# Kernel tuning notes

Hardware: AMD Instinct MI355X
Metric: run time of the kernel (lower is better)

## Reference

```python
import jax, jax.numpy as jnp
import numpy as np

DIM = 512
D_STATE = 16
D_CONV = 4
EXPAND = 2
D_INNER = EXPAND * DIM          # 1024
DT_RANK = (DIM + D_STATE - 1) // D_STATE  # 32
B_SZ, L_SEQ = 2, 2048


def layer_norm(x, w, b, eps=1e-5):
    mu = jnp.mean(x, axis=-1, keepdims=True)
    var = jnp.mean(jnp.square(x - mu), axis=-1, keepdims=True)
    return (x - mu) * jax.lax.rsqrt(var + eps) * w + b


def setup_inputs() -> dict:
    key = jax.random.key(0)
    ks = jax.random.split(key, 12)
    x = jax.random.normal(ks[0], (B_SZ, DIM, L_SEQ), dtype=jnp.float32)
    # LayerNorms init to weight=1, bias=0 per _init_weights
    norm1_w = jnp.ones((DIM,), jnp.float32)
    norm1_b = jnp.zeros((DIM,), jnp.float32)
    norm2_w = jnp.ones((DIM,), jnp.float32)
    norm2_b = jnp.zeros((DIM,), jnp.float32)
    # Mamba params (Linear weights trunc-normal std=0.02 per _init_weights; bias=0)
    in_proj_w = 0.02 * jax.random.truncated_normal(ks[1], -2., 2., (2 * D_INNER, DIM), jnp.float32)
    conv_w = 0.1 * jax.random.normal(ks[2], (D_INNER, D_CONV), jnp.float32)
    conv_b = jnp.zeros((D_INNER,), jnp.float32)
    x_proj_w = 0.02 * jax.random.truncated_normal(ks[3], -2., 2., (DT_RANK + 2 * D_STATE, D_INNER), jnp.float32)
    dt_proj_w = 0.02 * jax.random.truncated_normal(ks[4], -2., 2., (D_INNER, DT_RANK), jnp.float32)
    # dt bias: inverse-softplus of dt ~ U(1e-3, 0.1), standard Mamba init
    dt = jnp.exp(jax.random.uniform(ks[5], (D_INNER,), jnp.float32) * (np.log(0.1) - np.log(1e-3)) + np.log(1e-3))
    dt_proj_b = dt + jnp.log(-jnp.expm1(-dt))
    # S4D-real init: A = diag(1..d_state), stored as log
    A_log = jnp.log(jnp.broadcast_to(jnp.arange(1, D_STATE + 1, dtype=jnp.float32), (D_INNER, D_STATE)))
    D = jnp.ones((D_INNER,), jnp.float32)
    out_proj_w = 0.02 * jax.random.truncated_normal(ks[6], -2., 2., (DIM, D_INNER), jnp.float32)
    return {"x": x, "norm1_w": norm1_w, "norm1_b": norm1_b, "norm2_w": norm2_w,
            "norm2_b": norm2_b, "in_proj_w": in_proj_w, "conv_w": conv_w, "conv_b": conv_b,
            "x_proj_w": x_proj_w, "dt_proj_w": dt_proj_w, "dt_proj_b": dt_proj_b,
            "A_log": A_log, "D": D, "out_proj_w": out_proj_w}


def mamba_block(xn, in_proj_w, conv_w, conv_b, x_proj_w, dt_proj_w, dt_proj_b, A_log, D, out_proj_w):
    # xn: [B, L, dim]
    Bb, Ll, _ = xn.shape
    di = in_proj_w.shape[0] // 2
    xz = jnp.einsum('bld,ed->ble', xn, in_proj_w)          # [B, L, 2*di]
    x_in, z = xz[..., :di], xz[..., di:]
    # depthwise causal conv1d over L
    K = conv_w.shape[1]
    xp = jnp.pad(x_in, ((0, 0), (K - 1, 0), (0, 0)))
    xc = sum(xp[:, k:k + Ll, :] * conv_w[:, k] for k in range(K)) + conv_b
    xc = jax.nn.silu(xc)                                    # [B, L, di]
    # input-dependent dt, B, C
    dbl = jnp.einsum('bld,ed->ble', xc, x_proj_w)
    R, N = dt_proj_w.shape[1], A_log.shape[1]
    dt_lo, Bm, Cm = dbl[..., :R], dbl[..., R:R + N], dbl[..., R + N:]
    dt = jax.nn.softplus(jnp.einsum('blr,dr->bld', dt_lo, dt_proj_w) + dt_proj_b)  # [B, L, di]
    A = -jnp.exp(A_log)                                     # [di, N]
    dA = jnp.exp(jnp.einsum('bld,dn->bldn', dt, A))         # [B, L, di, N]
    dBu = jnp.einsum('bld,bln,bld->bldn', dt, Bm, xc)       # dt * B * u
    def step(h, inp):
        dA_t, dBu_t, C_t = inp                              # [B,di,N], [B,di,N], [B,N]
        h = dA_t * h + dBu_t
        y = jnp.einsum('bdn,bn->bd', h, C_t)
        return h, y
    h0 = jnp.zeros((Bb, di, N), xn.dtype)
    _, ys = jax.lax.scan(step, h0, (jnp.swapaxes(dA, 0, 1), jnp.swapaxes(dBu, 0, 1), jnp.swapaxes(Cm, 0, 1)))
    y = jnp.swapaxes(ys, 0, 1)                              # [B, L, di]
    y = y + xc * D
    y = y * jax.nn.silu(z)
    return jnp.einsum('ble,de->bld', y, out_proj_w)         # [B, L, dim]


def reference(x, norm1_w, norm1_b, norm2_w, norm2_b, in_proj_w, conv_w, conv_b,
              x_proj_w, dt_proj_w, dt_proj_b, A_log, D, out_proj_w):
    # x: [B, C, L]
    xf = jnp.swapaxes(x, 1, 2)                              # [B, L, C]
    xn = layer_norm(xf, norm1_w, norm1_b)
    xm = mamba_block(xn, in_proj_w, conv_w, conv_b, x_proj_w,
                     dt_proj_w, dt_proj_b, A_log, D, out_proj_w)
    out = layer_norm(xf + xm, norm2_w, norm2_b)
    return jnp.swapaxes(out, 1, 2)                          # [B, C, L]
```

## Files before the change

kernel.cpp:

```cpp
#include <hip/hip_runtime.h>
#include <math.h>

#define BSZ 2
#define LSEQ 2048
#define DMODEL 512
#define DINNER 1024
#define NST 16
#define RDT 32
#define GDBL 64
#define NCH 16
#define CHL 128
#define LOG2E 1.4426950408889634f

typedef unsigned short u16;
typedef unsigned int   u32;
typedef __attribute__((ext_vector_type(8))) __bf16 bf16x8;
typedef __attribute__((ext_vector_type(4))) float  f32x4;

__device__ __forceinline__ float siluf(float x){ return x / (1.f + __expf(-x)); }
__device__ __forceinline__ float softplusf(float x){
  return (x > 20.f) ? x : log1pf(__expf(x));
}
__device__ __forceinline__ u16 f2bf(float f){
  u32 u = __float_as_uint(f);
  u += 0x7fff + ((u >> 16) & 1);
  return (u16)(u >> 16);
}
__device__ __forceinline__ float bf2f(u16 u){ return __uint_as_float((u32)u << 16); }
__device__ __forceinline__ float exp2fast(float x){
  float r; asm("v_exp_f32 %0, %1" : "=v"(r) : "v"(x)); return r;
}
__device__ __forceinline__ void gld16(const void* g, void* l){
  __builtin_amdgcn_global_load_lds((const __attribute__((address_space(1))) void*)g,
                                   (__attribute__((address_space(3))) void*)l, 16, 0, 0);
}

__global__ void k0_wcvt(const float* __restrict__ Wip, const float* __restrict__ Wop,
                        const float* __restrict__ Wxp, const float* __restrict__ Wdt,
                        u16* __restrict__ wipb, u16* __restrict__ wopb,
                        u16* __restrict__ wxpb, u16* __restrict__ wdtb){
  int idx = blockIdx.x*256 + threadIdx.x;
  int i4 = idx * 4;
  const float* src; u16* dst;
  if (i4 < 1048576){ src = Wip + i4; dst = wipb + i4; }
  else if (i4 < 1048576 + 524288){ int j = i4 - 1048576; src = Wop + j; dst = wopb + j; }
  else if (i4 < 1048576 + 524288 + 65536){ int j = i4 - 1048576 - 524288; src = Wxp + j; dst = wxpb + j; }
  else { int j = i4 - 1048576 - 524288 - 65536; if (j >= 32768) return; src = Wdt + j; dst = wdtb + j; }
  float4 v = *(const float4*)src;
  u32 lo = (u32)f2bf(v.x) | ((u32)f2bf(v.y) << 16);
  u32 hi = (u32)f2bf(v.z) | ((u32)f2bf(v.w) << 16);
  *(uint2*)dst = make_uint2(lo, hi);
}

__global__ void k1_ln_norm(const float* __restrict__ x, const float* __restrict__ w1,
                           const float* __restrict__ b1, u16* __restrict__ xnb){
  int blk = blockIdx.x;
  int b = blk >> 6;
  int l0 = (blk & 63) * 32;
  int t = threadIdx.x;
  int lc = t & 31, dc = t >> 5;
  const float* xb = x + (size_t)b*DMODEL*LSEQ;
  float s=0.f, q=0.f;
  for (int d = dc*64; d < dc*64+64; ++d){
    float v = xb[d*LSEQ + l0 + lc];
    s += v; q += v*v;
  }
  __shared__ float ss[8][33], qq[8][33];
  __shared__ float muL[32], rsL[32];
  ss[dc][lc]=s; qq[dc][lc]=q;
  __syncthreads();
  if (t < 32){
    float S=0.f,Q=0.f;
    for (int i=0;i<8;++i){S+=ss[i][t];Q+=qq[i][t];}
    float m = S/DMODEL;
    muL[t]=m; rsL[t]=rsqrtf(Q/DMODEL - m*m + 1e-5f);
  }
  __syncthreads();
  float mu = muL[lc], rs = rsL[lc];
  u16* orow = xnb + ((size_t)(b*LSEQ + l0 + lc))*DMODEL;
  for (int d = dc*64; d < dc*64+64; d += 2){
    float v0 = (xb[d*LSEQ + l0 + lc]     - mu)*rs*w1[d]   + b1[d];
    float v1 = (xb[(d+1)*LSEQ + l0 + lc] - mu)*rs*w1[d+1] + b1[d+1];
    *(u32*)&orow[d] = (u32)f2bf(v0) | ((u32)f2bf(v1) << 16);
  }
}

__global__ __launch_bounds__(256) void k2_inproj_mfma(
    const u16* __restrict__ xnb, const u16* __restrict__ wipb,
    u16* __restrict__ xinb, u16* __restrict__ zb){
  __shared__ u16 As[2][4096];
  __shared__ u16 Bs[2][4096];
  int t = threadIdx.x;
  int wid = t >> 6, lane = t & 63;
  int n0 = blockIdx.x * 128, m0 = blockIdx.y * 128;
  int wr = wid >> 1, wc = wid & 1;
  int lr = lane & 15, q = lane >> 4;

  const u16* gA = xnb  + (size_t)(m0 + (t>>2))*DMODEL + (t&3)*8;
  const u16* gB = wipb + (size_t)(n0 + (t>>2))*DMODEL + (t&3)*8;

  f32x4 acc[4][4];
  #pragma unroll
  for (int i=0;i<4;++i)
    #pragma unroll
    for (int j=0;j<4;++j) acc[i][j] = (f32x4){0.f,0.f,0.f,0.f};

  #pragma unroll
  for (int r=0;r<2;++r){
    gld16(gA + (size_t)r*64*DMODEL, &As[0][(wid*64 + r*256)*8]);
    gld16(gB + (size_t)r*64*DMODEL, &Bs[0][(wid*64 + r*256)*8]);
  }
  const int abase = (wr*64 + lr)*32 + q*8;
  const int bbase = (wc*64 + lr)*32 + q*8;

  for (int ks = 0; ks < 16; ++ks){
    int cur = ks & 1;
    __syncthreads();
    if (ks < 15){
      const u16* gA2 = gA + (ks+1)*32;
      const u16* gB2 = gB + (ks+1)*32;
      #pragma unroll
      for (int r=0;r<2;++r){
        gld16(gA2 + (size_t)r*64*DMODEL, &As[cur^1][(wid*64 + r*256)*8]);
        gld16(gB2 + (size_t)r*64*DMODEL, &Bs[cur^1][(wid*64 + r*256)*8]);
      }
    }
    bf16x8 a[4], bv[4];
    #pragma unroll
    for (int mf=0; mf<4; ++mf) a[mf]  = *(const bf16x8*)&As[cur][abase + mf*512];
    #pragma unroll
    for (int nf=0; nf<4; ++nf) bv[nf] = *(const bf16x8*)&Bs[cur][bbase + nf*512];
    #pragma unroll
    for (int mf=0; mf<4; ++mf)
      #pragma unroll
      for (int nf=0; nf<4; ++nf)
        acc[mf][nf] = __builtin_amdgcn_mfma_f32_16x16x32_bf16(a[mf], bv[nf], acc[mf][nf], 0, 0, 0);
  }

  bool half = (n0 >= DINNER);
  u16* outp = half ? zb : xinb;
  int colb = (half ? n0 - DINNER : n0) + wc*64 + lr;
  #pragma unroll
  for (int mf=0; mf<4; ++mf){
    int rowb = m0 + wr*64 + mf*16 + q*4;
    #pragma unroll
    for (int nf=0; nf<4; ++nf){
      f32x4 v = acc[mf][nf];
      int col = colb + nf*16;
      #pragma unroll
      for (int j=0;j<4;++j) outp[(size_t)(rowb+j)*DINNER + col] = f2bf(v[j]);
    }
  }
}

__global__ void k3_conv(const u16* __restrict__ xinb, const float* __restrict__ cw,
                        const float* __restrict__ cb, u16* __restrict__ xc){
  int idx = blockIdx.x*blockDim.x + threadIdx.x;
  int e4 = (idx & (DINNER/4 - 1)) * 4;
  int m = idx >> 8;
  int b = m >> 11; int l = m & (LSEQ-1);
  float4 accb = *(const float4*)&cb[e4];
  float acc[4] = {accb.x, accb.y, accb.z, accb.w};
  #pragma unroll
  for (int k=0;k<4;++k){
    int li = l + k - 3;
    if (li >= 0){
      ushort4 v = *(const ushort4*)&xinb[((size_t)(b*LSEQ+li))*DINNER + e4];
      acc[0] += bf2f(v.x) * cw[(e4+0)*4 + k];
      acc[1] += bf2f(v.y) * cw[(e4+1)*4 + k];
      acc[2] += bf2f(v.z) * cw[(e4+2)*4 + k];
      acc[3] += bf2f(v.w) * cw[(e4+3)*4 + k];
    }
  }
  u32 lo = (u32)f2bf(siluf(acc[0])) | ((u32)f2bf(siluf(acc[1])) << 16);
  u32 hi = (u32)f2bf(siluf(acc[2])) | ((u32)f2bf(siluf(acc[3])) << 16);
  *(uint2*)&xc[(size_t)m*DINNER + e4] = make_uint2(lo, hi);
}

__global__ __launch_bounds__(256) void k4_xproj_mfma(
    const u16* __restrict__ xcbf, const u16* __restrict__ wxpb,
    float* __restrict__ dbl, u16* __restrict__ dtlob){
  __shared__ u16 As[2][4096];
  __shared__ u16 Bs[2][4096];
  int t = threadIdx.x;
  int wid = t >> 6, lane = t & 63;
  int m0 = blockIdx.x * 64;
  int wr = wid >> 1, wc = wid & 1;
  int lr = lane & 15, q = lane >> 4;

  const u16* gA = xcbf + (size_t)(m0 + (t>>2))*DINNER + (t&3)*8;
  const u16* gB = wxpb + (size_t)(t>>2)*DINNER + (t&3)*8;

  f32x4 acc[2][2];
  #pragma unroll
  for (int i=0;i<2;++i)
    #pragma unroll
    for (int j=0;j<2;++j) acc[i][j] = (f32x4){0.f,0.f,0.f,0.f};

  #pragma unroll
  for (int r=0;r<2;++r){
    gld16(gA + r*32, &As[0][(r*256 + wid*64)*8]);
    gld16(gB + r*32, &Bs[0][(r*256 + wid*64)*8]);
  }
  const int abase = (wr*32 + lr)*32 + q*8;
  const int bbase = (wc*32 + lr)*32 + q*8;

  for (int ks = 0; ks < 16; ++ks){
    int cur = ks & 1;
    __syncthreads();
    if (ks < 15){
      const u16* gA2 = gA + (ks+1)*64;
      const u16* gB2 = gB + (ks+1)*64;
      #pragma unroll
      for (int r=0;r<2;++r){
        gld16(gA2 + r*32, &As[cur^1][(r*256 + wid*64)*8]);
        gld16(gB2 + r*32, &Bs[cur^1][(r*256 + wid*64)*8]);
      }
    }
    bf16x8 a[2][2], bv[2][2];
    #pragma unroll
    for (int mf=0; mf<2; ++mf)
      #pragma unroll
      for (int s=0; s<2; ++s) a[mf][s] = *(const bf16x8*)&As[cur][abase + mf*512 + s*2048];
    #pragma unroll
    for (int nf=0; nf<2; ++nf)
      #pragma unroll
      for (int s=0; s<2; ++s) bv[nf][s] = *(const bf16x8*)&Bs[cur][bbase + nf*512 + s*2048];
    #pragma unroll
    for (int s=0; s<2; ++s)
      #pragma unroll
      for (int mf=0; mf<2; ++mf)
        #pragma unroll
        for (int nf=0; nf<2; ++nf)
          acc[mf][nf] = __builtin_amdgcn_mfma_f32_16x16x32_bf16(a[mf][s], bv[nf][s], acc[mf][nf], 0, 0, 0);
  }

  #pragma unroll
  for (int mf=0; mf<2; ++mf){
    int rowb = m0 + wr*32 + mf*16 + q*4;
    #pragma unroll
    for (int nf=0; nf<2; ++nf){
      f32x4 v = acc[mf][nf];
      int col = wc*32 + nf*16 + lr;
      #pragma unroll
      for (int j=0;j<4;++j) dbl[(size_t)(rowb+j)*GDBL + col] = v[j];
      if (wc == 0){
        #pragma unroll
        for (int j=0;j<4;++j) dtlob[(size_t)(rowb+j)*RDT + col] = f2bf(v[j]);
      }
    }
  }
}

__global__ __launch_bounds__(256) void k5_dtproj_mfma(
    const u16* __restrict__ dtlob, const u16* __restrict__ wdtb,
    const float* __restrict__ dtbias, u16* __restrict__ dtb){
  __shared__ u16 As[2048];
  __shared__ u16 Bs[2048];
  int t = threadIdx.x;
  int wid = t >> 6, lane = t & 63;
  int m0 = blockIdx.x * 64, d0 = blockIdx.y * 64;
  int wr = wid >> 1, wc = wid & 1;
  int lr = lane & 15, q = lane >> 4;

  gld16(dtlob + (size_t)(m0 + (t>>2))*RDT + (t&3)*8, &As[wid*512]);
  gld16(wdtb  + (size_t)(d0 + (t>>2))*RDT + (t&3)*8, &Bs[wid*512]);
  __syncthreads();

  f32x4 acc[2][2];
  bf16x8 a[2], bv[2];
  #pragma unroll
  for (int mf=0; mf<2; ++mf) a[mf]  = *(const bf16x8*)&As[(wr*32 + mf*16 + lr)*32 + q*8];
  #pragma unroll
  for (int nf=0; nf<2; ++nf) bv[nf] = *(const bf16x8*)&Bs[(wc*32 + nf*16 + lr)*32 + q*8];
  #pragma unroll
  for (int mf=0; mf<2; ++mf)
    #pragma unroll
    for (int nf=0; nf<2; ++nf)
      acc[mf][nf] = __builtin_amdgcn_mfma_f32_16x16x32_bf16(a[mf], bv[nf], (f32x4){0.f,0.f,0.f,0.f}, 0, 0, 0);

  #pragma unroll
  for (int nf=0; nf<2; ++nf){
    int col = d0 + wc*32 + nf*16 + lr;
    float bias = dtbias[col];
    #pragma unroll
    for (int mf=0; mf<2; ++mf){
      int rowb = m0 + wr*32 + mf*16 + q*4;
      f32x4 v = acc[mf][nf];
      #pragma unroll
      for (int j=0;j<4;++j) dtb[(size_t)(rowb+j)*DINNER + col] = f2bf(softplusf(v[j] + bias));
    }
  }
}

__global__ __launch_bounds__(256) void k6a_pass1(
    const float* __restrict__ dblg, const u16* __restrict__ xcg, const u16* __restrict__ dtg,
    const float* __restrict__ Alog,
    float* __restrict__ hend, float* __restrict__ dchunk){
  int blk = blockIdx.x;
  int b = blk >> 10;
  int slice = (blk >> 4) & 63;
  int chunk = blk & 15;
  int d0 = slice * 16;
  int t = threadIdx.x;
  int dl = t >> 4, n = t & 15;
  int d = d0 + dl;
  float Adn2 = -__expf(Alog[d*NST + n]) * LOG2E;
  float h = 0.f;
  float S = 0.f;

  __shared__ float dts_t[16][36];
  __shared__ float xcs_t[16][36];
  __shared__ float Bts[16][36];

  for (int sub = 0; sub < CHL/32; ++sub){
    int l0 = chunk*CHL + sub*32;
    __syncthreads();
    {
      int c = t & 15;
      int r1 = t >> 4, r2 = r1 + 16;
      size_t row1 = (size_t)(b*LSEQ + l0 + r1);
      size_t row2 = (size_t)(b*LSEQ + l0 + r2);
      dts_t[c][r1] = bf2f(dtg[row1*DINNER + d0 + c]);
      dts_t[c][r2] = bf2f(dtg[row2*DINNER + d0 + c]);
      xcs_t[c][r1] = bf2f(xcg[row1*DINNER + d0 + c]);
      xcs_t[c][r2] = bf2f(xcg[row2*DINNER + d0 + c]);
      Bts[c][r1]   = dblg[row1*GDBL + RDT + c];
      Bts[c][r2]   = dblg[row2*GDBL + RDT + c];
    }
    __syncthreads();
    for (int r0=0; r0<32; r0+=4){
      float4 dt4 = *(const float4*)&dts_t[dl][r0];
      float4 xc4 = *(const float4*)&xcs_t[dl][r0];
      float4 B4  = *(const float4*)&Bts[n][r0];
      const float* dtp = (const float*)&dt4;
      const float* xcp = (const float*)&xc4;
      const float* Bp  = (const float*)&B4;
      #pragma unroll
      for (int j=0;j<4;++j){
        float dtv = dtp[j];
        float a = exp2fast(dtv * Adn2);
        h = a*h + (dtv * xcp[j]) * Bp[j];
        S += dtv;
      }
    }
  }
  int cix = ((b*NCH + chunk)*DINNER + d)*NST + n;
  hend[cix]   = h;
  dchunk[cix] = exp2fast(Adn2 * S);
}

__global__ __launch_bounds__(256) void k6c_pass2(
    const float* __restrict__ dblg, const u16* __restrict__ xcg, const u16* __restrict__ zg,
    const u16* __restrict__ dtg,
    const float* __restrict__ Alog, const float* __restrict__ Dp,
    const float* __restrict__ hend, const float* __restrict__ dchk,
    u16* __restrict__ ybf){
  int blk = blockIdx.x;
  int b = blk >> 10;
  int slice = (blk >> 4) & 63;
  int chunk = blk & 15;
  int d0 = slice * 16;
  int t = threadIdx.x;
  int dl = t >> 4, n = t & 15;
  int d = d0 + dl;
  float Adn2 = -__expf(Alog[d*NST + n]) * LOG2E;

  float h = 0.f;
  {
    size_t base = ((size_t)(b*NCH) << 14) + (d<<4) + n;
    for (int c = 0; c < chunk; ++c){
      size_t ix = base + ((size_t)c << 14);
      h = dchk[ix]*h + hend[ix];
    }
  }

  __shared__ float dts_t[16][36];
  __shared__ float xcs_t[16][36];
  __shared__ float Bts[16][36];
  __shared__ float Cts[16][36];
  __shared__ float zs[32][17];
  __shared__ float ys[16][33];
  __shared__ float Dps[16];
  __shared__ float pbuf[32][260];

  if (t < 16) Dps[t] = Dp[d0+t];

  for (int sub = 0; sub < CHL/32; ++sub){
    int l0 = chunk*CHL + sub*32;
    __syncthreads();
    {
      int c = t & 15;
      int r1 = t >> 4, r2 = r1 + 16;
      size_t row1 = (size_t)(b*LSEQ + l0 + r1);
      size_t row2 = (size_t)(b*LSEQ + l0 + r2);
      dts_t[c][r1] = bf2f(dtg[row1*DINNER + d0 + c]);
      dts_t[c][r2] = bf2f(dtg[row2*DINNER + d0 + c]);
      xcs_t[c][r1] = bf2f(xcg[row1*DINNER + d0 + c]);
      xcs_t[c][r2] = bf2f(xcg[row2*DINNER + d0 + c]);
      Bts[c][r1]   = dblg[row1*GDBL + RDT + c];
      Bts[c][r2]   = dblg[row2*GDBL + RDT + c];
      Cts[c][r1]   = dblg[row1*GDBL + RDT + NST + c];
      Cts[c][r2]   = dblg[row2*GDBL + RDT + NST + c];
      zs[r1][c]    = bf2f(zg[row1*DINNER + d0 + c]);
      zs[r2][c]    = bf2f(zg[row2*DINNER + d0 + c]);
    }
    __syncthreads();
    for (int r0=0; r0<32; r0+=4){
      float4 dt4 = *(const float4*)&dts_t[dl][r0];
      float4 xc4 = *(const float4*)&xcs_t[dl][r0];
      float4 B4  = *(const float4*)&Bts[n][r0];
      float4 C4  = *(const float4*)&Cts[n][r0];
      const float* dtp = (const float*)&dt4;
      const float* xcp = (const float*)&xc4;
      const float* Bp  = (const float*)&B4;
      const float* Cp  = (const float*)&C4;
      #pragma unroll
      for (int j=0;j<4;++j){
        int r = r0 + j;
        float dtv = dtp[j];
        float a = exp2fast(dtv * Adn2);
        h = a*h + (dtv * xcp[j]) * Bp[j];
        pbuf[r][t ^ ((r&1)<<4)] = h * Cp[j];
      }
    }
    __syncthreads();
    {
      int rr_ = t & 31, dd_ = t >> 5;
      #pragma unroll
      for (int pp=0; pp<2; ++pp){
        int dd = dd_ + pp*8;
        int x0 = (dd*16) ^ ((rr_&1)<<4);
        float4 v0 = *(const float4*)&pbuf[rr_][x0 + 0];
        float4 v1 = *(const float4*)&pbuf[rr_][x0 + 4];
        float4 v2 = *(const float4*)&pbuf[rr_][x0 + 8];
        float4 v3 = *(const float4*)&pbuf[rr_][x0 + 12];
        float sum = (((v0.x+v0.y)+(v0.z+v0.w)) + ((v1.x+v1.y)+(v1.z+v1.w)))
                  + (((v2.x+v2.y)+(v2.z+v2.w)) + ((v3.x+v3.y)+(v3.z+v3.w)));
        float xv = xcs_t[dd][rr_];
        float zv = zs[rr_][dd];
        ys[dd][rr_] = (sum + xv*Dps[dd]) * siluf(zv);
      }
    }
    __syncthreads();
    {
      int r = t >> 3, pr = t & 7;
      float v0 = ys[pr*2][r];
      float v1 = ys[pr*2+1][r];
      u32 u = (u32)f2bf(v0) | ((u32)f2bf(v1) << 16);
      *(u32*)&ybf[((size_t)(b*LSEQ + l0 + r))*DINNER + d0 + pr*2] = u;
    }
  }
}

__global__ __launch_bounds__(256) void k7_outproj_mfma(
    const u16* __restrict__ ybf, const u16* __restrict__ wopb, float* __restrict__ xmT){
  __shared__ u16 As[2][4096];
  __shared__ u16 Bs[2][4096];
  int t = threadIdx.x;
  int wid = t >> 6, lane = t & 63;
  int n0 = blockIdx.x * 64, m0 = blockIdx.y * 64;
  int b  = m0 >> 11;
  int l0 = m0 & (LSEQ-1);
  int wr = wid >> 1, wc = wid & 1;
  int lr = lane & 15, q = lane >> 4;

  const u16* gA = ybf  + (size_t)(m0 + (t>>2))*DINNER + (t&3)*8;
  const u16* gB = wopb + (size_t)(n0 + (t>>2))*DINNER + (t&3)*8;

  f32x4 acc[2][2];
  #pragma unroll
  for (int i=0;i<2;++i)
    #pragma unroll
    for (int j=0;j<2;++j) acc[i][j] = (f32x4){0.f,0.f,0.f,0.f};

  #pragma unroll
  for (int r=0;r<2;++r){
    gld16(gA + r*32, &As[0][(r*256 + wid*64)*8]);
    gld16(gB + r*32, &Bs[0][(r*256 + wid*64)*8]);
  }
  const int abase = (wr*32 + lr)*32 + q*8;
  const int bbase = (wc*32 + lr)*32 + q*8;

  for (int ks = 0; ks < 16; ++ks){
    int cur = ks & 1;
    __syncthreads();
    if (ks < 15){
      const u16* gA2 = gA + (ks+1)*64;
      const u16* gB2 = gB + (ks+1)*64;
      #pragma unroll
      for (int r=0;r<2;++r){
        gld16(gA2 + r*32, &As[cur^1][(r*256 + wid*64)*8]);
        gld16(gB2 + r*32, &Bs[cur^1][(r*256 + wid*64)*8]);
      }
    }
    bf16x8 a[2][2], bv[2][2];
    #pragma unroll
    for (int mf=0; mf<2; ++mf)
      #pragma unroll
      for (int s=0; s<2; ++s) a[mf][s] = *(const bf16x8*)&As[cur][abase + mf*512 + s*2048];
    #pragma unroll
    for (int nf=0; nf<2; ++nf)
      #pragma unroll
      for (int s=0; s<2; ++s) bv[nf][s] = *(const bf16x8*)&Bs[cur][bbase + nf*512 + s*2048];
    #pragma unroll
    for (int s=0; s<2; ++s)
      #pragma unroll
      for (int mf=0; mf<2; ++mf)
        #pragma unroll
        for (int nf=0; nf<2; ++nf)
          acc[mf][nf] = __builtin_amdgcn_mfma_f32_16x16x32_bf16(a[mf][s], bv[nf][s], acc[mf][nf], 0, 0, 0);
  }

  #pragma unroll
  for (int mf=0; mf<2; ++mf){
    int lrow = l0 + wr*32 + mf*16 + q*4;
    #pragma unroll
    for (int nf=0; nf<2; ++nf){
      f32x4 v = acc[mf][nf];
      int col = n0 + wc*32 + nf*16 + lr;
      *(float4*)&xmT[((size_t)(b*DMODEL + col))*LSEQ + lrow] = make_float4(v[0],v[1],v[2],v[3]);
    }
  }
}

__global__ void k8_fused(const float* __restrict__ x, const float* __restrict__ xmT,
                         const float* __restrict__ w2, const float* __restrict__ b2,
                         float* __restrict__ out){
  int blk = blockIdx.x;
  int b = blk >> 7;
  int l0 = (blk & 127) * 16;
  int t = threadIdx.x;
  int lc = t & 15, dc = t >> 4;
  const float* xb = x   + (size_t)b*DMODEL*LSEQ + l0 + lc;
  const float* xt = xmT + (size_t)b*DMODEL*LSEQ + l0 + lc;
  float s=0.f, q=0.f;
  for (int d = dc*32; d < dc*32+32; ++d){
    float v = xb[d*LSEQ] + xt[d*LSEQ];
    s += v; q += v*v;
  }
  __shared__ float ss[16][17], qq[16][17];
  __shared__ float muL[16], rsL[16];
  ss[dc][lc]=s; qq[dc][lc]=q;
  __syncthreads();
  if (t < 16){
    float S=0.f,Q=0.f;
    for (int i=0;i<16;++i){S+=ss[i][t];Q+=qq[i][t];}
    float m = S/DMODEL;
    muL[t]=m; rsL[t]=rsqrtf(Q/DMODEL - m*m + 1e-5f);
  }
  __syncthreads();
  float mu = muL[lc], rs = rsL[lc];
  float* ob = out + (size_t)b*DMODEL*LSEQ + l0 + lc;
  for (int d = dc*32; d < dc*32+32; ++d){
    float v = xb[d*LSEQ] + xt[d*LSEQ];
    ob[d*LSEQ] = (v - mu)*rs*w2[d] + b2[d];
  }
}

extern "C" void kernel_launch(void* const* d_in, const int* in_sizes, int n_in,
                              void* d_out, int out_size, void* d_ws, size_t ws_size,
                              hipStream_t stream) {
  const float* x      = (const float*)d_in[0];
  const float* n1w    = (const float*)d_in[1];
  const float* n1b    = (const float*)d_in[2];
  const float* n2w    = (const float*)d_in[3];
  const float* n2b    = (const float*)d_in[4];
  const float* Wip    = (const float*)d_in[5];
  const float* cw     = (const float*)d_in[6];
  const float* cb     = (const float*)d_in[7];
  const float* Wxp    = (const float*)d_in[8];
  const float* Wdt    = (const float*)d_in[9];
  const float* dtbias = (const float*)d_in[10];
  const float* Alog   = (const float*)d_in[11];
  const float* Dp     = (const float*)d_in[12];
  const float* Wop    = (const float*)d_in[13];
  float* out = (float*)d_out;

  float* ws = (float*)d_ws;
  size_t o = 0;
  u16*  xinb = (u16*)(ws + o); o += 2097152;
  u16*  zb   = (u16*)(ws + o); o += 2097152;
  u16*  xcb  = (u16*)(ws + o); o += 2097152;
  u16*  ybf  = (u16*)(ws + o); o += 2097152;
  u16*  dtb  = (u16*)(ws + o); o += 2097152;
  u16*  xnb  = (u16*)(ws + o); o += 1048576;
  u16*  wipb = (u16*)(ws + o); o += 524288;
  u16*  wopb = (u16*)(ws + o); o += 262144;
  u16*  wxpb = (u16*)(ws + o); o += 32768;
  u16*  wdtb = (u16*)(ws + o); o += 16384;
  u16*  dtlob= (u16*)(ws + o); o += 65536;
  float* dbl  = ws + o; o += 262144;
  float* hend = ws + o; o += 524288;
  float* dchk = ws + o; o += 524288;
  float* xmT  = ws + o; o += 2097152;

  k0_wcvt      <<<dim3(1632),        dim3(256), 0, stream>>>(Wip, Wop, Wxp, Wdt, wipb, wopb, wxpb, wdtb);
  k1_ln_norm   <<<dim3(BSZ*64),      dim3(256), 0, stream>>>(x, n1w, n1b, xnb);
  k2_inproj_mfma<<<dim3(16,32),      dim3(256), 0, stream>>>(xnb, wipb, xinb, zb);
  k3_conv      <<<dim3(4096),        dim3(256), 0, stream>>>(xinb, cw, cb, xcb);
  k4_xproj_mfma<<<dim3(64),          dim3(256), 0, stream>>>(xcb, wxpb, dbl, dtlob);
  k5_dtproj_mfma<<<dim3(64,16),      dim3(256), 0, stream>>>(dtlob, wdtb, dtbias, dtb);
  k6a_pass1    <<<dim3(BSZ*64*NCH),  dim3(256), 0, stream>>>(dbl, xcb, dtb, Alog, hend, dchk);
  k6c_pass2    <<<dim3(BSZ*64*NCH),  dim3(256), 0, stream>>>(dbl, xcb, zb, dtb, Alog, Dp, hend, dchk, ybf);
  k7_outproj_mfma<<<dim3(8,64),      dim3(256), 0, stream>>>(ybf, wopb, xmT);
  k8_fused     <<<dim3(BSZ*128),     dim3(256), 0, stream>>>(x, xmT, n2w, n2b, out);
}
```

Baseline: 182.8 us.

## Remap selective scan to four states per thread with vectorized loads and DPP reduction

The two chunked-scan kernels now give each thread four state channels for one inner channel and cover 64 channels per block instead of 16. Chunk length is halved, so there are twice as many chunks. Tiles are loaded as 16-byte bf16 vectors into row-major shared memory. The C-weighted sum over states is reduced with DPP quad shuffles instead of a large shared partial-sum buffer, and the output is written as vectorized bf16. This aims to cut transposed scalar global loads, shared-memory traffic and barriers per step. In exchange, the serial cross-chunk carry loop in pass 2 gets longer and the hend/dchk buffers double in size.

New measurement: 165.1 us. 9.6% less time.

```diff
diff --git a/kernel.cpp b/kernel.cpp
--- a/kernel.cpp
+++ b/kernel.cpp
@@ -8,8 +8,8 @@
 #define NST 16
 #define RDT 32
 #define GDBL 64
-#define NCH 16
-#define CHL 128
+#define NCH 32
+#define CHL 64
 #define LOG2E 1.4426950408889634f
 
 typedef unsigned short u16;
@@ -33,6 +33,17 @@
 __device__ __forceinline__ void gld16(const void* g, void* l){
   __builtin_amdgcn_global_load_lds((const __attribute__((address_space(1))) void*)g,
                                    (__attribute__((address_space(3))) void*)l, 16, 0, 0);
+}
+__device__ __forceinline__ void unpack8(uint4 v, float* f){
+  f[0]=__uint_as_float(v.x<<16); f[1]=__uint_as_float(v.x&0xffff0000u);
+  f[2]=__uint_as_float(v.y<<16); f[3]=__uint_as_float(v.y&0xffff0000u);
+  f[4]=__uint_as_float(v.z<<16); f[5]=__uint_as_float(v.z&0xffff0000u);
+  f[6]=__uint_as_float(v.w<<16); f[7]=__uint_as_float(v.w&0xffff0000u);
+}
+__device__ __forceinline__ float quadsum(float p){
+  p += __int_as_float(__builtin_amdgcn_update_dpp(0, __float_as_int(p), 0xB1, 0xf, 0xf, true));
+  p += __int_as_float(__builtin_amdgcn_update_dpp(0, __float_as_int(p), 0x4E, 0xf, 0xf, true));
+  return p;
 }
 
 __global__ void k0_wcvt(const float* __restrict__ Wip, const float* __restrict__ Wop,
@@ -298,56 +309,62 @@
     const float* __restrict__ Alog,
     float* __restrict__ hend, float* __restrict__ dchunk){
   int blk = blockIdx.x;
-  int b = blk >> 10;
-  int slice = (blk >> 4) & 63;
-  int chunk = blk & 15;
-  int d0 = slice * 16;
-  int t = threadIdx.x;
-  int dl = t >> 4, n = t & 15;
-  int d = d0 + dl;
-  float Adn2 = -__expf(Alog[d*NST + n]) * LOG2E;
-  float h = 0.f;
-  float S = 0.f;
-
-  __shared__ float dts_t[16][36];
-  __shared__ float xcs_t[16][36];
-  __shared__ float Bts[16][36];
+  int b = blk >> 9;
+  int dblk = (blk >> 5) & 15;
+  int chunk = blk & 31;
+  int d0 = dblk * 64;
+  int t = threadIdx.x;
+  int d = t >> 2, ng = t & 3;
+
+  float4 Adn2;
+  {
+    float4 al = *(const float4*)&Alog[(d0+d)*NST + ng*4];
+    Adn2.x = -__expf(al.x)*LOG2E; Adn2.y = -__expf(al.y)*LOG2E;
+    Adn2.z = -__expf(al.z)*LOG2E; Adn2.w = -__expf(al.w)*LOG2E;
+  }
+  float h0=0.f, h1=0.f, h2=0.f, h3=0.f, S=0.f;
+
+  __shared__ float dts[32][64];
+  __shared__ float xcs[32][64];
+  __shared__ float Bst[32][16];
 
   for (int sub = 0; sub < CHL/32; ++sub){
     int l0 = chunk*CHL + sub*32;
     __syncthreads();
     {
-      int c = t & 15;
-      int r1 = t >> 4, r2 = r1 + 16;
-      size_t row1 = (size_t)(b*LSEQ + l0 + r1);
-      size_t row2 = (size_t)(b*LSEQ + l0 + r2);
-      dts_t[c][r1] = bf2f(dtg[row1*DINNER + d0 + c]);
-      dts_t[c][r2] = bf2f(dtg[row2*DINNER + d0 + c]);
-      xcs_t[c][r1] = bf2f(xcg[row1*DINNER + d0 + c]);
-      xcs_t[c][r2] = bf2f(xcg[row2*DINNER + d0 + c]);
-      Bts[c][r1]   = dblg[row1*GDBL + RDT + c];
-      Bts[c][r2]   = dblg[row2*GDBL + RDT + c];
-    }
-    __syncthreads();
-    for (int r0=0; r0<32; r0+=4){
-      float4 dt4 = *(const float4*)&dts_t[dl][r0];
-      float4 xc4 = *(const float4*)&xcs_t[dl][r0];
-      float4 B4  = *(const float4*)&Bts[n][r0];
-      const float* dtp = (const float*)&dt4;
-      const float* xcp = (const float*)&xc4;
-      const float* Bp  = (const float*)&B4;
-      #pragma unroll
-      for (int j=0;j<4;++j){
-        float dtv = dtp[j];
-        float a = exp2fast(dtv * Adn2);
-        h = a*h + (dtv * xcp[j]) * Bp[j];
-        S += dtv;
+      int r = t >> 3, c8 = t & 7;
+      size_t row = (size_t)(b*LSEQ + l0 + r);
+      uint4 dv = *(const uint4*)&dtg[row*DINNER + d0 + c8*8];
+      uint4 xv = *(const uint4*)&xcg[row*DINNER + d0 + c8*8];
+      float df[8], xf[8];
+      unpack8(dv, df); unpack8(xv, xf);
+      *(float4*)&dts[r][c8*8]   = make_float4(df[0],df[1],df[2],df[3]);
+      *(float4*)&dts[r][c8*8+4] = make_float4(df[4],df[5],df[6],df[7]);
+      *(float4*)&xcs[r][c8*8]   = make_float4(xf[0],xf[1],xf[2],xf[3]);
+      *(float4*)&xcs[r][c8*8+4] = make_float4(xf[4],xf[5],xf[6],xf[7]);
+      if (t < 128){
+        int rB = t >> 2, qB = t & 3;
+        *(float4*)&Bst[rB][qB*4] = *(const float4*)&dblg[((size_t)(b*LSEQ + l0 + rB))*GDBL + RDT + qB*4];
       }
     }
-  }
-  int cix = ((b*NCH + chunk)*DINNER + d)*NST + n;
-  hend[cix]   = h;
-  dchunk[cix] = exp2fast(Adn2 * S);
+    __syncthreads();
+    #pragma unroll 4
+    for (int r = 0; r < 32; ++r){
+      float dtv = dts[r][d];
+      float xcv = xcs[r][d];
+      float4 Bv = *(const float4*)&Bst[r][ng*4];
+      float u = dtv * xcv;
+      h0 = exp2fast(dtv*Adn2.x)*h0 + u*Bv.x;
+      h1 = exp2fast(dtv*Adn2.y)*h1 + u*Bv.y;
+      h2 = exp2fast(dtv*Adn2.z)*h2 + u*Bv.z;
+      h3 = exp2fast(dtv*Adn2.w)*h3 + u*Bv.w;
+      S += dtv;
+    }
+  }
+  size_t cix = ((size_t)(b*NCH + chunk)*DINNER + d0 + d)*NST + ng*4;
+  *(float4*)&hend[cix]   = make_float4(h0, h1, h2, h3);
+  *(float4*)&dchunk[cix] = make_float4(exp2fast(Adn2.x*S), exp2fast(Adn2.y*S),
+                                       exp2fast(Adn2.z*S), exp2fast(Adn2.w*S));
 }
 
 __global__ __launch_bounds__(256) void k6c_pass2(
@@ -357,98 +374,98 @@
     const float* __restrict__ hend, const float* __restrict__ dchk,
     u16* __restrict__ ybf){
   int blk = blockIdx.x;
-  int b = blk >> 10;
-  int slice = (blk >> 4) & 63;
-  int chunk = blk & 15;
-  int d0 = slice * 16;
-  int t = threadIdx.x;
-  int dl = t >> 4, n = t & 15;
-  int d = d0 + dl;
-  float Adn2 = -__expf(Alog[d*NST + n]) * LOG2E;
-
-  float h = 0.f;
+  int b = blk >> 9;
+  int dblk = (blk >> 5) & 15;
+  int chunk = blk & 31;
+  int d0 = dblk * 64;
+  int t = threadIdx.x;
+  int d = t >> 2, ng = t & 3;
+
+  float4 Adn2;
   {
-    size_t base = ((size_t)(b*NCH) << 14) + (d<<4) + n;
+    float4 al = *(const float4*)&Alog[(d0+d)*NST + ng*4];
+    Adn2.x = -__expf(al.x)*LOG2E; Adn2.y = -__expf(al.y)*LOG2E;
+    Adn2.z = -__expf(al.z)*LOG2E; Adn2.w = -__expf(al.w)*LOG2E;
+  }
+
+  float h0=0.f, h1=0.f, h2=0.f, h3=0.f;
+  {
+    size_t base = ((size_t)(b*NCH)*DINNER + d0 + d)*NST + ng*4;
     for (int c = 0; c < chunk; ++c){
-      size_t ix = base + ((size_t)c << 14);
-      h = dchk[ix]*h + hend[ix];
-    }
-  }
-
-  __shared__ float dts_t[16][36];
-  __shared__ float xcs_t[16][36];
-  __shared__ float Bts[16][36];
-  __shared__ float Cts[16][36];
-  __shared__ float zs[32][17];
-  __shared__ float ys[16][33];
-  __shared__ float Dps[16];
-  __shared__ float pbuf[32][260];
-
-  if (t < 16) Dps[t] = Dp[d0+t];
+      size_t ix = base + (size_t)c*DINNER*NST;
+      float4 hv = *(const float4*)&hend[ix];
+      float4 dv = *(const float4*)&dchk[ix];
+      h0 = dv.x*h0 + hv.x; h1 = dv.y*h1 + hv.y;
+      h2 = dv.z*h2 + hv.z; h3 = dv.w*h3 + hv.w;
+    }
+  }
+
+  __shared__ float dts[32][64];
+  __shared__ float xcs[32][64];
+  __shared__ float BCs[32][32];
+  __shared__ float ys[32][64];
+  __shared__ float Dps[64];
+
+  if (t < 64) Dps[t] = Dp[d0 + t];
 
   for (int sub = 0; sub < CHL/32; ++sub){
     int l0 = chunk*CHL + sub*32;
     __syncthreads();
     {
-      int c = t & 15;
-      int r1 = t >> 4, r2 = r1 + 16;
-      size_t row1 = (size_t)(b*LSEQ + l0 + r1);
-      size_t row2 = (size_t)(b*LSEQ + l0 + r2);
-      dts_t[c][r1] = bf2f(dtg[row1*DINNER + d0 + c]);
-      dts_t[c][r2] = bf2f(dtg[row2*DINNER + d0 + c]);
-      xcs_t[c][r1] = bf2f(xcg[row1*DINNER + d0 + c]);
-      xcs_t[c][r2] = bf2f(xcg[row2*DINNER + d0 + c]);
-      Bts[c][r1]   = dblg[row1*GDBL + RDT + c];
-      Bts[c][r2]   = dblg[row2*GDBL + RDT + c];
-      Cts[c][r1]   = dblg[row1*GDBL + RDT + NST + c];
-      Cts[c][r2]   = dblg[row2*GDBL + RDT + NST + c];
-      zs[r1][c]    = bf2f(zg[row1*DINNER + d0 + c]);
-      zs[r2][c]    = bf2f(zg[row2*DINNER + d0 + c]);
-    }
-    __syncthreads();
-    for (int r0=0; r0<32; r0+=4){
-      float4 dt4 = *(const float4*)&dts_t[dl][r0];
-      float4 xc4 = *(const float4*)&xcs_t[dl][r0];
-      float4 B4  = *(const float4*)&Bts[n][r0];
-      float4 C4  = *(const float4*)&Cts[n][r0];
-      const float* dtp = (const float*)&dt4;
-      const float* xcp = (const float*)&xc4;
-      const float* Bp  = (const float*)&B4;
-      const float* Cp  = (const float*)&C4;
-      #pragma unroll
-      for (int j=0;j<4;++j){
-        int r = r0 + j;
-        float dtv = dtp[j];
-        float a = exp2fast(dtv * Adn2);
-        h = a*h + (dtv * xcp[j]) * Bp[j];
-        pbuf[r][t ^ ((r&1)<<4)] = h * Cp[j];
-      }
+      int r = t >> 3, c8 = t & 7;
+      size_t row = (size_t)(b*LSEQ + l0 + r);
+      uint4 dv = *(const uint4*)&dtg[row*DINNER + d0 + c8*8];
+      uint4 xv = *(const uint4*)&xcg[row*DINNER + d0 + c8*8];
+      float df[8], xf[8];
+      unpack8(dv, df); unpack8(xv, xf);
+      *(float4*)&dts[r][c8*8]   = make_float4(df[0],df[1],df[2],df[3]);
+      *(float4*)&dts[r][c8*8+4] = make_float4(df[4],df[5],df[6],df[7]);
+      *(float4*)&xcs[r][c8*8]   = make_float4(xf[0],xf[1],xf[2],xf[3]);
+      *(float4*)&xcs[r][c8*8+4] = make_float4(xf[4],xf[5],xf[6],xf[7]);
+      *(float4*)&BCs[r][c8*4]   = *(const float4*)&dblg[row*GDBL + RDT + c8*4];
+    }
+    __syncthreads();
+    #pragma unroll 4
+    for (int r = 0; r < 32; ++r){
+      float dtv = dts[r][d];
+      float xcv = xcs[r][d];
+      float4 Bv = *(const float4*)&BCs[r][ng*4];
+      float4 Cv = *(const float4*)&BCs[r][16 + ng*4];
+      float u = dtv * xcv;
+      h0 = exp2fast(dtv*Adn2.x)*h0 + u*Bv.x;
+      h1 = exp2fast(dtv*Adn2.y)*h1 + u*Bv.y;
+      h2 = exp2fast(dtv*Adn2.z)*h2 + u*Bv.z;
+      h3 = exp2fast(dtv*Adn2.w)*h3 + u*Bv.w;
+      float p = h0*Cv.x + h1*Cv.y + h2*Cv.z + h3*Cv.w;
+      p = quadsum(p);
+      if (ng == 0) ys[r][d] = p;
     }
     __syncthreads();
     {
-      int rr_ = t & 31, dd_ = t >> 5;
-      #pragma unroll
-      for (int pp=0; pp<2; ++pp){
-        int dd = dd_ + pp*8;
-        int x0 = (dd*16) ^ ((rr_&1)<<4);
-        float4 v0 = *(const float4*)&pbuf[rr_][x0 + 0];
-        float4 v1 = *(const float4*)&pbuf[rr_][x0 + 4];
-        float4 v2 = *(const float4*)&pbuf[rr_][x0 + 8];
-        float4 v3 = *(const float4*)&pbuf[rr_][x0 + 12];
-        float sum = (((v0.x+v0.y)+(v0.z+v0.w)) + ((v1.x+v1.y)+(v1.z+v1.w)))
-                  + (((v2.x+v2.y)+(v2.z+v2.w)) + ((v3.x+v3.y)+(v3.z+v3.w)));
-        float xv = xcs_t[dd][rr_];
-        float zv = zs[rr_][dd];
-        ys[dd][rr_] = (sum + xv*Dps[dd]) * siluf(zv);
-      }
-    }
-    __syncthreads();
-    {
-      int r = t >> 3, pr = t & 7;
-      float v0 = ys[pr*2][r];
-      float v1 = ys[pr*2+1][r];
-      u32 u = (u32)f2bf(v0) | ((u32)f2bf(v1) << 16);
-      *(u32*)&ybf[((size_t)(b*LSEQ + l0 + r))*DINNER + d0 + pr*2] = u;
+      int r = t >> 3, c8 = t & 7;
+      size_t row = (size_t)(b*LSEQ + l0 + r);
+      uint4 zv = *(const uint4*)&zg[row*DINNER + d0 + c8*8];
+      float zf[8]; unpack8(zv, zf);
+      float4 s0 = *(const float4*)&ys[r][c8*8];
+      float4 s1 = *(const float4*)&ys[r][c8*8+4];
+      float4 x0 = *(const float4*)&xcs[r][c8*8];
+      float4 x1 = *(const float4*)&xcs[r][c8*8+4];
+      float4 D0 = *(const float4*)&Dps[c8*8];
+      float4 D1 = *(const float4*)&Dps[c8*8+4];
+      float y0 = (s0.x + x0.x*D0.x)*siluf(zf[0]);
+      float y1 = (s0.y + x0.y*D0.y)*siluf(zf[1]);
+      float y2 = (s0.z + x0.z*D0.z)*siluf(zf[2]);
+      float y3 = (s0.w + x0.w*D0.w)*siluf(zf[3]);
+      float y4 = (s1.x + x1.x*D1.x)*siluf(zf[4]);
+      float y5 = (s1.y + x1.y*D1.y)*siluf(zf[5]);
+      float y6 = (s1.z + x1.z*D1.z)*siluf(zf[6]);
+      float y7 = (s1.w + x1.w*D1.w)*siluf(zf[7]);
+      uint4 o;
+      o.x = (u32)f2bf(y0) | ((u32)f2bf(y1) << 16);
+      o.y = (u32)f2bf(y2) | ((u32)f2bf(y3) << 16);
+      o.z = (u32)f2bf(y4) | ((u32)f2bf(y5) << 16);
+      o.w = (u32)f2bf(y6) | ((u32)f2bf(y7) << 16);
+      *(uint4*)&ybf[row*DINNER + d0 + c8*8] = o;
     }
   }
 }
@@ -591,8 +608,8 @@
   u16*  wdtb = (u16*)(ws + o); o += 16384;
   u16*  dtlob= (u16*)(ws + o); o += 65536;
   float* dbl  = ws + o; o += 262144;
-  float* hend = ws + o; o += 524288;
-  float* dchk = ws + o; o += 524288;
+  float* hend = ws + o; o += 1048576;
+  float* dchk = ws + o; o += 1048576;
   float* xmT  = ws + o; o += 2097152;
 
   k0_wcvt      <<<dim3(1632),        dim3(256), 0, stream>>>(Wip, Wop, Wxp, Wdt, wipb, wopb, wxpb, wdtb);
@@ -601,8 +618,8 @@
   k3_conv      <<<dim3(4096),        dim3(256), 0, stream>>>(xinb, cw, cb, xcb);
   k4_xproj_mfma<<<dim3(64),          dim3(256), 0, stream>>>(xcb, wxpb, dbl, dtlob);
   k5_dtproj_mfma<<<dim3(64,16),      dim3(256), 0, stream>>>(dtlob, wdtb, dtbias, dtb);
-  k6a_pass1    <<<dim3(BSZ*64*NCH),  dim3(256), 0, stream>>>(dbl, xcb, dtb, Alog, hend, dchk);
-  k6c_pass2    <<<dim3(BSZ*64*NCH),  dim3(256), 0, stream>>>(dbl, xcb, zb, dtb, Alog, Dp, hend, dchk, ybf);
+  k6a_pass1    <<<dim3(BSZ*16*NCH),  dim3(256), 0, stream>>>(dbl, xcb, dtb, Alog, hend, dchk);
+  k6c_pass2    <<<dim3(BSZ*16*NCH),  dim3(256), 0, stream>>>(dbl, xcb, zb, dtb, Alog, Dp, hend, dchk, ybf);
   k7_outproj_mfma<<<dim3(8,64),      dim3(256), 0, stream>>>(ybf, wopb, xmT);
   k8_fused     <<<dim3(BSZ*128),     dim3(256), 0, stream>>>(x, xmT, n2w, n2b, out);
 }
```
